# Kernel optimization log

Measured on AMD Instinct MI355X. Metric: run time of the kernel, lower is better.

## Reference

```python
import jax, jax.numpy as jnp
import numpy as np

CH = 64
CF = CH // 8  # f/g projection channels


def setup_inputs() -> dict:
    key = jax.random.key(0)
    k1, k2, k3, k4, k5 = jax.random.split(key, 5)
    x = jax.random.normal(k1, (8, 64, 64, CH), dtype=jnp.float32)
    kernel_f = 0.02 * jax.random.normal(k2, (1, 1, CH, CF), dtype=jnp.float32)
    kernel_g = 0.02 * jax.random.normal(k3, (1, 1, CH, CF), dtype=jnp.float32)
    kernel_h = 0.02 * jax.random.normal(k4, (1, 1, CH, CH), dtype=jnp.float32)
    gamma = 0.02 * jax.random.normal(k5, (1,), dtype=jnp.float32)
    return {"x": x, "kernel_f": kernel_f, "kernel_g": kernel_g,
            "kernel_h": kernel_h, "gamma": gamma}


def reference(x, kernel_f, kernel_g, kernel_h, gamma):
    B, H, W, C = x.shape
    N = H * W
    xf = x.reshape(B, N, C)  # flatten spatial; 1x1 conv == matmul over channels
    f = jnp.einsum('bnc,cd->bnd', xf, kernel_f[0, 0])  # [B,N,CF]
    g = jnp.einsum('bnc,cd->bnd', xf, kernel_g[0, 0])  # [B,N,CF]
    h = jnp.einsum('bnc,cd->bnd', xf, kernel_h[0, 0])  # [B,N,C]
    s = jnp.einsum('bnd,bmd->bnm', g, f)  # g @ f^T, [B,N,N]
    beta = jax.nn.softmax(s, axis=-1)
    o = jnp.einsum('bnm,bmc->bnc', beta, h)  # [B,N,C]
    out = gamma * o.reshape(B, H, W, C) + x
    return out
```

## Files before the change

### kernel.cpp

```cpp
#include <hip/hip_runtime.h>
#include <hip/hip_bf16.h>

typedef __attribute__((ext_vector_type(4)))  float f32x4;
typedef __attribute__((ext_vector_type(16))) float f32x16;
typedef __attribute__((ext_vector_type(8)))  short bf16x8;

#define LOG2E 1.44269504088896340736f

#if __has_builtin(__builtin_amdgcn_exp2f)
static __device__ __forceinline__ float exp2_native(float x) {
  return __builtin_amdgcn_exp2f(x);
}
#else
extern "C" __device__ float __ocml_native_exp2_f32(float);
static __device__ __forceinline__ float exp2_native(float x) {
  return __ocml_native_exp2_f32(x);
}
#endif

static __device__ __forceinline__ unsigned int pack_trunc_f(float a, float b) {
  return __builtin_amdgcn_perm(__float_as_uint(b), __float_as_uint(a), 0x07060302);
}

typedef const __attribute__((address_space(1))) unsigned int gu32;
typedef __attribute__((address_space(3))) unsigned int lu32;
static __device__ __forceinline__ void gload_lds16(const void* g, void* l) {
  __builtin_amdgcn_global_load_lds((gu32*)g, (lu32*)l, 16, 0, 0);
}

__global__ __launch_bounds__(256) void proj_kernel(
    const float* __restrict__ x, const float* __restrict__ kf,
    const float* __restrict__ kg, const float* __restrict__ kh,
    unsigned short* __restrict__ f_b, unsigned short* __restrict__ g_b,
    unsigned short* __restrict__ h_p)
{
  __shared__ unsigned short Kt[80*72];
  const int t = threadIdx.x, blk = blockIdx.x;

  #pragma unroll
  for (int r = 0; r < 20; ++r) {
    int idx = r*256 + t;
    int o = idx >> 6, c = idx & 63;
    float v = (o < 8) ? kf[c*8 + o]
            : (o < 16) ? kg[c*8 + (o-8)] * LOG2E
            : kh[c*64 + (o-16)];
    Kt[o*72 + c] = (unsigned short)(__float_as_uint(v) >> 16);
  }
  __syncthreads();

  const int w = t >> 6, lane = t & 63, l15 = lane & 15, quad = lane >> 4;
  const int Rbase = blk*64 + w*16;
  const int R = Rbase + l15;

  bf16x8 af[2];
  #pragma unroll
  for (int kk = 0; kk < 2; ++kk) {
    const float* xp = x + (long)R*64 + kk*32 + quad*8;
    float4 v0 = *(const float4*)xp;
    float4 v1 = *(const float4*)(xp + 4);
    union { unsigned int u[4]; bf16x8 v; } p;
    p.u[0] = pack_trunc_f(v0.x, v0.y);
    p.u[1] = pack_trunc_f(v0.z, v0.w);
    p.u[2] = pack_trunc_f(v1.x, v1.y);
    p.u[3] = pack_trunc_f(v1.z, v1.w);
    af[kk] = p.v;
  }

  f32x4 acc[5];
  #pragma unroll
  for (int nt = 0; nt < 5; ++nt) { f32x4 z = {}; acc[nt] = z; }

  #pragma unroll
  for (int nt = 0; nt < 5; ++nt)
    #pragma unroll
    for (int kk = 0; kk < 2; ++kk) {
      bf16x8 bfv = *(const bf16x8*)&Kt[(nt*16 + l15)*72 + kk*32 + quad*8];
      acc[nt] = __builtin_amdgcn_mfma_f32_16x16x32_bf16(af[kk], bfv, acc[nt], 0, 0, 0);
    }

  const int bt = Rbase >> 12;
  const int kt = (Rbase >> 7) & 31;
  const int base = ((blk & 1) << 6) + (w << 4);
  const int pi = base + ((quad & 1) << 3) + (((quad >> 1) & 1) << 2);

  #pragma unroll
  for (int rr = 0; rr < 4; ++rr) {
    const int nq = (Rbase + quad*4 + rr) & 4095;
    unsigned short v = (unsigned short)(__float_as_uint(acc[0][rr]) >> 16);
    if (l15 < 8) f_b[((long)bt*4096 + nq)*8 + l15] = v;
    else         g_b[((long)bt*4096 + nq)*8 + (l15 - 8)] = v;
  }
  #pragma unroll
  for (int nt = 1; nt < 5; ++nt) {
    const int c = (nt - 1)*16 + l15;
    uint2 v;
    v.x = pack_trunc_f(acc[nt][0], acc[nt][1]);
    v.y = pack_trunc_f(acc[nt][2], acc[nt][3]);
    *(uint2*)(h_p + ((long)(bt*32 + kt)*64 + c)*136 + pi) = v;
  }
}

__global__ __launch_bounds__(128, 2) void attn_kernel(
    const unsigned short* __restrict__ f_b, const unsigned short* __restrict__ g_b,
    const unsigned short* __restrict__ h_p, unsigned short* __restrict__ po,
    float* __restrict__ pl)
{
  __shared__ unsigned short bufs[2][9728];

  const int t = threadIdx.x;
  const int w = t >> 6, lane = t & 63, l31 = lane & 31, a = lane >> 5;
  const int qb = blockIdx.x, b = blockIdx.y, sp = blockIdx.z;
  const int q0w = qb*128 + w*64;

  bf16x8 gf[2];
  #pragma unroll
  for (int qg = 0; qg < 2; ++qg) {
    bf16x8 gv = *(const bf16x8*)(g_b + ((long)b*4096 + q0w + qg*32 + l31)*8);
    bf16x8 z = {};
    gf[qg] = (a == 0) ? gv : z;
  }

  f32x16 oacc[2][2];
  { f32x16 z = {}; oacc[0][0] = z; oacc[0][1] = z; oacc[1][0] = z; oacc[1][1] = z; }
  float l_run[2] = {0.f, 0.f};

  const char* hp_b = (const char*)h_p + (long)b*32*17408;
  const char* fb_b = (const char*)f_b + (long)b*4096*16;

  auto stage = [&](int bi, int kt) {
    const char* hsrc = hp_b + (long)kt*17408;
    const char* fsrc = fb_b + (long)kt*2048;
    char* dst = (char*)&bufs[bi][0];
    #pragma unroll
    for (int i = 0; i < 8; ++i)
      gload_lds16(hsrc + i*2048 + w*1024 + lane*16, dst + i*2048 + w*1024);
    if (w == 0) {
      gload_lds16(hsrc + 16384 + lane*16, dst + 16384);
    } else {
      gload_lds16(fsrc + lane*16,        dst + 17408);
      gload_lds16(fsrc + 1024 + lane*16, dst + 17408 + 1024);
    }
  };

  stage(0, sp*8);

  for (int ktl = 0; ktl < 8; ++ktl) {
    __syncthreads();
    if (ktl < 7) stage((ktl + 1) & 1, sp*8 + ktl + 1);

    const unsigned short* hts = &bufs[ktl & 1][0];
    const unsigned short* fts = &bufs[ktl & 1][8704];

    #pragma unroll
    for (int mt = 0; mt < 4; ++mt) {
      bf16x8 afv = *(const bf16x8*)&fts[(mt*32 + l31)*8];
      f32x16 zz = {};
      f32x16 sc0 = __builtin_amdgcn_mfma_f32_32x32x16_bf16(afv, gf[0], zz, 0, 0, 0);
      f32x16 sc1 = __builtin_amdgcn_mfma_f32_32x32x16_bf16(afv, gf[1], zz, 0, 0, 0);

      float e0[16], e1[16];
      #pragma unroll
      for (int r = 0; r < 16; ++r) {
        e0[r] = exp2_native(sc0[r]);
        e1[r] = exp2_native(sc1[r]);
        l_run[0] += e0[r];
        l_run[1] += e1[r];
      }

      #pragma unroll
      for (int half = 0; half < 2; ++half) {
        const int s = mt*2 + half;
        bf16x8 bh0 = *(const bf16x8*)&hts[(l31)*136      + s*16 + a*8];
        bf16x8 bh1 = *(const bf16x8*)&hts[(32 + l31)*136 + s*16 + a*8];
        union { unsigned int u[4]; bf16x8 v; } ap0, ap1;
        #pragma unroll
        for (int j = 0; j < 4; ++j) {
          ap0.u[j] = pack_trunc_f(e0[half*8 + 2*j], e0[half*8 + 2*j + 1]);
          ap1.u[j] = pack_trunc_f(e1[half*8 + 2*j], e1[half*8 + 2*j + 1]);
        }
        oacc[0][0] = __builtin_amdgcn_mfma_f32_32x32x16_bf16(ap0.v, bh0, oacc[0][0], 0, 0, 0);
        oacc[0][1] = __builtin_amdgcn_mfma_f32_32x32x16_bf16(ap0.v, bh1, oacc[0][1], 0, 0, 0);
        oacc[1][0] = __builtin_amdgcn_mfma_f32_32x32x16_bf16(ap1.v, bh0, oacc[1][0], 0, 0, 0);
        oacc[1][1] = __builtin_amdgcn_mfma_f32_32x32x16_bf16(ap1.v, bh1, oacc[1][1], 0, 0, 0);
      }
    }
  }

  const long sb = (long)sp*8 + b;
  #pragma unroll
  for (int qg = 0; qg < 2; ++qg) {
    float l = l_run[qg] + __shfl_xor(l_run[qg], 32);
    if (lane < 32) pl[(sb << 12) + q0w + qg*32 + l31] = l;
    unsigned short* pob = po + ((sb << 12) + q0w + qg*32)*64;
    #pragma unroll
    for (int nt = 0; nt < 2; ++nt)
      #pragma unroll
      for (int r = 0; r < 16; ++r) {
        const int q = (r & 3) + 8*(r >> 2) + 4*a;
        pob[(long)q*64 + nt*32 + l31] =
            (unsigned short)(__float_as_uint(oacc[qg][nt][r]) >> 16);
      }
  }
}

__global__ __launch_bounds__(256) void combine_kernel(
    const float* __restrict__ x, const unsigned short* __restrict__ po,
    const float* __restrict__ pl, const float* __restrict__ gamma_p,
    float* __restrict__ out)
{
  const long tid = (long)blockIdx.x*256 + threadIdx.x;
  const long bn = tid >> 3;
  const int c0 = (int)(tid & 7)*8;

  float l = 0.f;
  float o[8];
  #pragma unroll
  for (int i = 0; i < 8; ++i) o[i] = 0.f;
  #pragma unroll
  for (int s = 0; s < 4; ++s) {
    l += pl[(long)s*32768 + bn];
    uint4 v = *(const uint4*)(po + ((long)s*32768 + bn)*64 + c0);
    const unsigned short* pv = (const unsigned short*)&v;
    #pragma unroll
    for (int i = 0; i < 8; ++i)
      o[i] += __uint_as_float((unsigned int)pv[i] << 16);
  }
  const float scale = gamma_p[0] / l;
  const float* xp = x + bn*64 + c0;
  float4 x0 = *(const float4*)xp;
  float4 x1 = *(const float4*)(xp + 4);
  float4 r0, r1;
  r0.x = fmaf(scale, o[0], x0.x);
  r0.y = fmaf(scale, o[1], x0.y);
  r0.z = fmaf(scale, o[2], x0.z);
  r0.w = fmaf(scale, o[3], x0.w);
  r1.x = fmaf(scale, o[4], x1.x);
  r1.y = fmaf(scale, o[5], x1.y);
  r1.z = fmaf(scale, o[6], x1.z);
  r1.w = fmaf(scale, o[7], x1.w);
  float* op = out + bn*64 + c0;
  *(float4*)op = r0;
  *(float4*)(op + 4) = r1;
}

extern "C" void kernel_launch(void* const* d_in, const int* in_sizes, int n_in,
                              void* d_out, int out_size, void* d_ws, size_t ws_size,
                              hipStream_t stream) {
  const float* x  = (const float*)d_in[0];
  const float* kf = (const float*)d_in[1];
  const float* kg = (const float*)d_in[2];
  const float* kh = (const float*)d_in[3];
  const float* gamma = (const float*)d_in[4];
  float* out = (float*)d_out;

  char* ws = (char*)d_ws;
  unsigned short* h_p = (unsigned short*)ws;
  unsigned short* f_b = (unsigned short*)(ws + 4456448);
  unsigned short* g_b = (unsigned short*)(ws + 4980736);
  unsigned short* po  = (unsigned short*)(ws + 5505024);
  float*          pl  = (float*)(ws + 22282240);

  proj_kernel<<<512, 256, 0, stream>>>(x, kf, kg, kh, f_b, g_b, h_p);
  attn_kernel<<<dim3(32, 8, 4), 128, 0, stream>>>(f_b, g_b, h_p, po, pl);
  combine_kernel<<<1024, 256, 0, stream>>>(x, po, pl, gamma, out);
}
```

Before: 102.7 us.

## Halve attention key tile and double KV split count for more parallelism

Shrinks each attention stage's key tile from 128 to 64 keys, with a new h_p layout (row stride 68 instead of 136), and doubles the split-K factor from 4 to 8, so there are twice as many attention blocks. With the smaller LDS footprint, launch bounds allow 4 blocks per SM instead of 2. The aim is better occupancy and load balance on the attention kernel. The cost is more partial outputs for the combine kernel to read and sum, and a larger workspace. The exp loop also now reuses the score registers and splits the row-sum accumulation into two partial sums to shorten the dependency chain.

After: 255.4 us. +148.7%, slower.

```diff
diff --git a/kernel.cpp b/kernel.cpp
--- a/kernel.cpp
+++ b/kernel.cpp
@@ -78,10 +78,9 @@
       acc[nt] = __builtin_amdgcn_mfma_f32_16x16x32_bf16(af[kk], bfv, acc[nt], 0, 0, 0);
     }
 
-  const int bt = Rbase >> 12;
-  const int kt = (Rbase >> 7) & 31;
-  const int base = ((blk & 1) << 6) + (w << 4);
-  const int pi = base + ((quad & 1) << 3) + (((quad >> 1) & 1) << 2);
+  const int bt = blk >> 6;
+  const int kt64 = blk & 63;
+  const int pi = (w << 4) + ((quad & 1) << 3) + (((quad >> 1) & 1) << 2);
 
   #pragma unroll
   for (int rr = 0; rr < 4; ++rr) {
@@ -96,16 +95,16 @@
     uint2 v;
     v.x = pack_trunc_f(acc[nt][0], acc[nt][1]);
     v.y = pack_trunc_f(acc[nt][2], acc[nt][3]);
-    *(uint2*)(h_p + ((long)(bt*32 + kt)*64 + c)*136 + pi) = v;
-  }
-}
-
-__global__ __launch_bounds__(128, 2) void attn_kernel(
+    *(uint2*)(h_p + (long)(bt*64 + kt64)*4608 + c*68 + pi) = v;
+  }
+}
+
+__global__ __launch_bounds__(128, 4) void attn_kernel(
     const unsigned short* __restrict__ f_b, const unsigned short* __restrict__ g_b,
     const unsigned short* __restrict__ h_p, unsigned short* __restrict__ po,
     float* __restrict__ pl)
 {
-  __shared__ unsigned short bufs[2][9728];
+  __shared__ char bufs[2][10240];
 
   const int t = threadIdx.x;
   const int w = t >> 6, lane = t & 63, l31 = lane & 31, a = lane >> 5;
@@ -124,21 +123,18 @@
   { f32x16 z = {}; oacc[0][0] = z; oacc[0][1] = z; oacc[1][0] = z; oacc[1][1] = z; }
   float l_run[2] = {0.f, 0.f};
 
-  const char* hp_b = (const char*)h_p + (long)b*32*17408;
+  const char* hp_b = (const char*)h_p + (long)b*64*9216;
   const char* fb_b = (const char*)f_b + (long)b*4096*16;
 
-  auto stage = [&](int bi, int kt) {
-    const char* hsrc = hp_b + (long)kt*17408;
-    const char* fsrc = fb_b + (long)kt*2048;
-    char* dst = (char*)&bufs[bi][0];
-    #pragma unroll
-    for (int i = 0; i < 8; ++i)
-      gload_lds16(hsrc + i*2048 + w*1024 + lane*16, dst + i*2048 + w*1024);
-    if (w == 0) {
-      gload_lds16(hsrc + 16384 + lane*16, dst + 16384);
-    } else {
-      gload_lds16(fsrc + lane*16,        dst + 17408);
-      gload_lds16(fsrc + 1024 + lane*16, dst + 17408 + 1024);
+  auto stage = [&](int bi, int kt64) {
+    const char* hsrc = hp_b + (long)kt64*9216;
+    const char* fsrc = fb_b + (long)kt64*1024;
+    char* dst = &bufs[bi][0];
+    #pragma unroll
+    for (int i = 0; i < 5; ++i) {
+      const int o = i*2048 + w*1024;
+      const char* src = (o < 9216) ? (hsrc + o) : (fsrc + (o - 9216));
+      gload_lds16(src + lane*16, dst + o);
     }
   };
 
@@ -148,35 +144,39 @@
     __syncthreads();
     if (ktl < 7) stage((ktl + 1) & 1, sp*8 + ktl + 1);
 
-    const unsigned short* hts = &bufs[ktl & 1][0];
-    const unsigned short* fts = &bufs[ktl & 1][8704];
-
-    #pragma unroll
-    for (int mt = 0; mt < 4; ++mt) {
+    const unsigned short* hts = (const unsigned short*)&bufs[ktl & 1][0];
+    const unsigned short* fts = (const unsigned short*)&bufs[ktl & 1][9216];
+
+    #pragma unroll
+    for (int mt = 0; mt < 2; ++mt) {
       bf16x8 afv = *(const bf16x8*)&fts[(mt*32 + l31)*8];
       f32x16 zz = {};
       f32x16 sc0 = __builtin_amdgcn_mfma_f32_32x32x16_bf16(afv, gf[0], zz, 0, 0, 0);
       f32x16 sc1 = __builtin_amdgcn_mfma_f32_32x32x16_bf16(afv, gf[1], zz, 0, 0, 0);
 
-      float e0[16], e1[16];
+      float la0 = 0.f, lb0 = 0.f, la1 = 0.f, lb1 = 0.f;
       #pragma unroll
-      for (int r = 0; r < 16; ++r) {
-        e0[r] = exp2_native(sc0[r]);
-        e1[r] = exp2_native(sc1[r]);
-        l_run[0] += e0[r];
-        l_run[1] += e1[r];
+      for (int r = 0; r < 16; r += 2) {
+        sc0[r]   = exp2_native(sc0[r]);
+        sc0[r+1] = exp2_native(sc0[r+1]);
+        sc1[r]   = exp2_native(sc1[r]);
+        sc1[r+1] = exp2_native(sc1[r+1]);
+        la0 += sc0[r]; lb0 += sc0[r+1];
+        la1 += sc1[r]; lb1 += sc1[r+1];
       }
+      l_run[0] += la0 + lb0;
+      l_run[1] += la1 + lb1;
 
       #pragma unroll
       for (int half = 0; half < 2; ++half) {
         const int s = mt*2 + half;
-        bf16x8 bh0 = *(const bf16x8*)&hts[(l31)*136      + s*16 + a*8];
-        bf16x8 bh1 = *(const bf16x8*)&hts[(32 + l31)*136 + s*16 + a*8];
+        bf16x8 bh0 = *(const bf16x8*)&hts[(l31)*68      + s*16 + a*8];
+        bf16x8 bh1 = *(const bf16x8*)&hts[(32 + l31)*68 + s*16 + a*8];
         union { unsigned int u[4]; bf16x8 v; } ap0, ap1;
         #pragma unroll
         for (int j = 0; j < 4; ++j) {
-          ap0.u[j] = pack_trunc_f(e0[half*8 + 2*j], e0[half*8 + 2*j + 1]);
-          ap1.u[j] = pack_trunc_f(e1[half*8 + 2*j], e1[half*8 + 2*j + 1]);
+          ap0.u[j] = pack_trunc_f(sc0[half*8 + 2*j], sc0[half*8 + 2*j + 1]);
+          ap1.u[j] = pack_trunc_f(sc1[half*8 + 2*j], sc1[half*8 + 2*j + 1]);
         }
         oacc[0][0] = __builtin_amdgcn_mfma_f32_32x32x16_bf16(ap0.v, bh0, oacc[0][0], 0, 0, 0);
         oacc[0][1] = __builtin_amdgcn_mfma_f32_32x32x16_bf16(ap0.v, bh1, oacc[0][1], 0, 0, 0);
@@ -217,7 +217,7 @@
   #pragma unroll
   for (int i = 0; i < 8; ++i) o[i] = 0.f;
   #pragma unroll
-  for (int s = 0; s < 4; ++s) {
+  for (int s = 0; s < 8; ++s) {
     l += pl[(long)s*32768 + bn];
     uint4 v = *(const uint4*)(po + ((long)s*32768 + bn)*64 + c0);
     const unsigned short* pv = (const unsigned short*)&v;
@@ -255,12 +255,12 @@
 
   char* ws = (char*)d_ws;
   unsigned short* h_p = (unsigned short*)ws;
-  unsigned short* f_b = (unsigned short*)(ws + 4456448);
-  unsigned short* g_b = (unsigned short*)(ws + 4980736);
-  unsigned short* po  = (unsigned short*)(ws + 5505024);
-  float*          pl  = (float*)(ws + 22282240);
+  unsigned short* f_b = (unsigned short*)(ws + 4718592);
+  unsigned short* g_b = (unsigned short*)(ws + 5242880);
+  unsigned short* po  = (unsigned short*)(ws + 5767168);
+  float*          pl  = (float*)(ws + 39321600);
 
   proj_kernel<<<512, 256, 0, stream>>>(x, kf, kg, kh, f_b, g_b, h_p);
-  attn_kernel<<<dim3(32, 8, 4), 128, 0, stream>>>(f_b, g_b, h_p, po, pl);
+  attn_kernel<<<dim3(32, 8, 8), 128, 0, stream>>>(f_b, g_b, h_p, po, pl);
   combine_kernel<<<1024, 256, 0, stream>>>(x, po, pl, gamma, out);
 }
```
